# Optimization experiments

Measured on AMD Instinct MI355X. Metric: run time of the kernel, lower is better.

The kernel has to match this reference:

```python
import jax, jax.numpy as jnp
import numpy as np

N_NODES = 100000


def setup_inputs() -> dict:
    key = jax.random.key(0)
    ks = jax.random.split(key, 4)
    x = jax.random.normal(ks[0], (N_NODES, 128), dtype=jnp.float32)
    edge_index = jax.random.randint(ks[1], (2, 1600000), 0, N_NODES, dtype=jnp.int64)
    W1 = jax.random.normal(ks[2], (128, 64), dtype=jnp.float32) * (1.0 / np.sqrt(128))
    b1 = jnp.zeros((64,), dtype=jnp.float32)
    W2 = jax.random.normal(ks[3], (64, 64), dtype=jnp.float32) * (1.0 / np.sqrt(64))
    b2 = jnp.zeros((64,), dtype=jnp.float32)
    return {"x": x, "edge_index": edge_index, "W1": W1, "b1": b1, "W2": W2, "b2": b2}


def reference(x, edge_index, W1, b1, W2, b2):
    N = x.shape[0]
    loop = jnp.arange(N, dtype=edge_index.dtype)
    src = jnp.concatenate([edge_index[0], loop])  # [E+N] sources (incl. self-loops)
    dst = jnp.concatenate([edge_index[1], loop])  # [E+N] targets
    # symmetric GCN normalization: deg counts edge weights (all 1) at target nodes
    deg = jax.ops.segment_sum(jnp.ones_like(src, dtype=x.dtype), dst, num_segments=N)
    dinv = jnp.where(deg > 0, jax.lax.rsqrt(deg), 0.0)
    norm = (dinv[src] * dinv[dst])[:, None]  # [E+N, 1]

    def gcn_conv(h, W, b):
        h = h @ W                                   # dense transform [N, out]
        msg = h[src] * norm                         # gather + normalize [E+N, out]
        agg = jax.ops.segment_sum(msg, dst, num_segments=N)  # scatter-add
        return agg + b

    h = jax.nn.gelu(gcn_conv(x, W1, b1), approximate=False)  # torch nn.GELU = exact erf
    return gcn_conv(h, W2, b2)
```

## Files before the change

kernel.cpp:

```cpp
#include <hip/hip_runtime.h>
#include <math.h>

#define N_NODES 100000
#define N_EDGES 1600000
#define NROWS 100032
#define NBUK 782
#define BCAP 2600
#define BINCHUNK 4096

typedef unsigned short u16;
typedef u16 u16x4 __attribute__((ext_vector_type(4)));
typedef u16 u16x8 __attribute__((ext_vector_type(8)));
typedef short s16x8 __attribute__((ext_vector_type(8)));
typedef float f32x4 __attribute__((ext_vector_type(4)));

__device__ __forceinline__ float bf2f(u16 u) {
    union { unsigned i; float f; } v; v.i = ((unsigned)u) << 16; return v.f;
}
__device__ __forceinline__ u16 f2bf(float f) {
    union { float f; unsigned i; } v; v.f = f;
    return (u16)((v.i + 0x7FFFu + ((v.i >> 16) & 1u)) >> 16);
}

__global__ __launch_bounds__(256) void k_bin(const int* __restrict__ src,
                                             const int* __restrict__ dst,
                                             int* bucketCursor,
                                             unsigned int* __restrict__ bins) {
    __shared__ int lcnt[NBUK];
    __shared__ int lbase[NBUK];
    const int t = threadIdx.x;
    for (int i = t; i < NBUK; i += 256) lcnt[i] = 0;
    __syncthreads();

    const int e0 = blockIdx.x * BINCHUNK + t * 16;
    int4 s4[4], d4[4];
    int bkt[16], rnk[16];
    const bool valid = e0 < N_EDGES;
    if (valid) {
        #pragma unroll
        for (int k = 0; k < 4; ++k) {
            s4[k] = *(const int4*)(src + e0 + 4 * k);
            d4[k] = *(const int4*)(dst + e0 + 4 * k);
        }
        #pragma unroll
        for (int k = 0; k < 4; ++k) {
            int dd[4] = { d4[k].x, d4[k].y, d4[k].z, d4[k].w };
            #pragma unroll
            for (int j = 0; j < 4; ++j) {
                int b = dd[j] >> 7;
                bkt[4 * k + j] = b;
                rnk[4 * k + j] = atomicAdd(&lcnt[b], 1);
            }
        }
    }
    __syncthreads();
    for (int i = t; i < NBUK; i += 256)
        if (lcnt[i] > 0) lbase[i] = atomicAdd(&bucketCursor[i], lcnt[i]);
    __syncthreads();
    if (valid) {
        #pragma unroll
        for (int k = 0; k < 4; ++k) {
            int ss[4] = { s4[k].x, s4[k].y, s4[k].z, s4[k].w };
            int dd[4] = { d4[k].x, d4[k].y, d4[k].z, d4[k].w };
            #pragma unroll
            for (int j = 0; j < 4; ++j) {
                int i = 4 * k + j;
                unsigned w = ((unsigned)(dd[j] & 127) << 17) | (unsigned)ss[j];
                bins[(size_t)bkt[i] * BCAP + lbase[bkt[i]] + rnk[i]] = w;
            }
        }
    }
}

__global__ __launch_bounds__(256) void k_bscan(const int* __restrict__ bucketCursor,
                                               int* __restrict__ gBase,
                                               int* __restrict__ row_start) {
    __shared__ int sd[256];
    const int t = threadIdx.x;
    const int idx0 = t * 4;
    int v0 = (idx0 + 0 < NBUK) ? bucketCursor[idx0 + 0] : 0;
    int v1 = (idx0 + 1 < NBUK) ? bucketCursor[idx0 + 1] : 0;
    int v2 = (idx0 + 2 < NBUK) ? bucketCursor[idx0 + 2] : 0;
    int v3 = (idx0 + 3 < NBUK) ? bucketCursor[idx0 + 3] : 0;
    int s0 = v0, s1 = s0 + v1, s2 = s1 + v2, s3 = s2 + v3;
    sd[t] = s3;
    __syncthreads();
    #pragma unroll
    for (int off = 1; off < 256; off <<= 1) {
        int x = (t >= off) ? sd[t - off] : 0;
        __syncthreads();
        sd[t] += x;
        __syncthreads();
    }
    int excl = (t > 0) ? sd[t - 1] : 0;
    if (idx0 + 0 < NBUK) gBase[idx0 + 0] = excl;
    if (idx0 + 1 < NBUK) gBase[idx0 + 1] = excl + s0;
    if (idx0 + 2 < NBUK) gBase[idx0 + 2] = excl + s1;
    if (idx0 + 3 < NBUK) gBase[idx0 + 3] = excl + s2;
    if (t == 0) row_start[N_NODES] = N_EDGES;
}

__global__ __launch_bounds__(256) void k_build(const unsigned int* __restrict__ bins,
                                               const int* __restrict__ bucketCursor,
                                               const int* __restrict__ gBase,
                                               int* __restrict__ row_start,
                                               float* __restrict__ dinv,
                                               int* __restrict__ csr_src) {
    __shared__ int cnt[128];
    __shared__ int ps[128];
    __shared__ int cur[128];
    const int b = blockIdx.x;
    const int t = threadIdx.x;
    const int bcnt = bucketCursor[b];
    const int gb = gBase[b];
    const unsigned int* mybins = bins + (size_t)b * BCAP;

    if (t < 128) cnt[t] = 0;
    __syncthreads();
    for (int i = t; i < bcnt; i += 256)
        atomicAdd(&cnt[mybins[i] >> 17], 1);
    __syncthreads();
    if (t < 128) ps[t] = cnt[t];
    __syncthreads();
    #pragma unroll
    for (int off = 1; off < 128; off <<= 1) {
        int x = (t >= off && t < 128) ? ps[t - off] : 0;
        __syncthreads();
        if (t < 128) ps[t] += x;
        __syncthreads();
    }
    if (t < 128) {
        int excl = (t > 0) ? ps[t - 1] : 0;
        cur[t] = excl;
        int node = (b << 7) + t;
        if (node < N_NODES) {
            row_start[node] = gb + excl;
            dinv[node] = rsqrtf((float)(cnt[t] + 1));
        }
    }
    __syncthreads();
    for (int i = t; i < bcnt; i += 256) {
        unsigned w = mybins[i];
        int dl = w >> 17;
        int s = (int)(w & 0x1FFFFu);
        int p = atomicAdd(&cur[dl], 1);
        csr_src[gb + p] = s;
    }
}

__global__ __launch_bounds__(256) void k_wsplit(const float* __restrict__ W1,
                                                const float* __restrict__ W2,
                                                u16* __restrict__ w1pre,
                                                u16* __restrict__ w2pre) {
    const int t = threadIdx.x;
    const int b = blockIdx.x;
    if (b < 16) {
        #pragma unroll
        for (int half = 0; half < 2; ++half) {
            int e = b * 512 + half * 256 + t;
            int k = e >> 6, c = e & 63;
            float f = W1[e];
            u16 h = f2bf(f);
            u16 l = f2bf(f - bf2f(h));
            int byte = (c * 256 + k * 2) ^ ((c & 7) << 4);
            *(u16*)((char*)w1pre + byte) = h;
            *(u16*)((char*)w1pre + 16384 + byte) = l;
        }
    } else {
        int e = (b - 16) * 256 + t;
        int k = e >> 6, c = e & 63;
        float f = W2[e];
        u16 h = f2bf(f);
        u16 l = f2bf(f - bf2f(h));
        int byte = (c * 128 + k * 2) ^ ((c & 7) << 4);
        *(u16*)((char*)w2pre + byte) = h;
        *(u16*)((char*)w2pre + 8192 + byte) = l;
    }
}

__device__ __forceinline__ void quant_store_row(float v0, float v1, float v2, float v3,
                                                int row, int l16,
                                                signed char* __restrict__ H8,
                                                float* __restrict__ scale) {
    float m = fmaxf(fmaxf(fabsf(v0), fabsf(v1)), fmaxf(fabsf(v2), fabsf(v3)));
    m = fmaxf(m, __shfl_xor(m, 1));
    m = fmaxf(m, __shfl_xor(m, 2));
    m = fmaxf(m, __shfl_xor(m, 4));
    m = fmaxf(m, __shfl_xor(m, 8));
    float inv = (m > 0.f) ? 127.f / m : 0.f;
    if (l16 == 0) scale[row] = m * (1.f / 127.f);
    size_t base = (size_t)row * 64 + l16;
    H8[base +  0] = (signed char)__float2int_rn(v0 * inv);
    H8[base + 16] = (signed char)__float2int_rn(v1 * inv);
    H8[base + 32] = (signed char)__float2int_rn(v2 * inv);
    H8[base + 48] = (signed char)__float2int_rn(v3 * inv);
}

__global__ __launch_bounds__(256) void k_gemm1(const float* __restrict__ X,
                                               const u16* __restrict__ w1pre,
                                               const float* __restrict__ dinv,
                                               signed char* __restrict__ H8,
                                               float* __restrict__ scale) {
    __shared__ u16 sxh[64 * 128];
    __shared__ u16 sxl[64 * 128];
    __shared__ u16 wth[64 * 128];
    __shared__ u16 wtl[64 * 128];
    const int t = threadIdx.x;
    const int blk = blockIdx.x;

    {
        const float4* Xv = (const float4*)X;
        #pragma unroll
        for (int i = 0; i < 8; ++i) {
            int idx = i * 256 + t;
            int row = idx >> 5;
            int k4  = (idx & 31) << 2;
            int grow = blk * 64 + row;
            float4 v = make_float4(0.f, 0.f, 0.f, 0.f);
            if (grow < N_NODES) v = Xv[(size_t)grow * 32 + (idx & 31)];
            float f[4] = { v.x, v.y, v.z, v.w };
            u16x4 hv, lv;
            #pragma unroll
            for (int j = 0; j < 4; ++j) {
                u16 h = f2bf(f[j]);
                hv[j] = h;
                lv[j] = f2bf(f[j] - bf2f(h));
            }
            int byte = (row * 256 + k4 * 2) ^ ((row & 7) << 4);
            *(u16x4*)((char*)sxh + byte) = hv;
            *(u16x4*)((char*)sxl + byte) = lv;
        }
    }
    {
        const u16x8* G = (const u16x8*)w1pre;
        u16x8* Lh = (u16x8*)wth;
        u16x8* Ll = (u16x8*)wtl;
        #pragma unroll
        for (int i = 0; i < 4; ++i) Lh[i * 256 + t] = G[i * 256 + t];
        #pragma unroll
        for (int i = 0; i < 4; ++i) Ll[i * 256 + t] = G[1024 + i * 256 + t];
    }
    __syncthreads();

    const int lane = t & 63;
    const int w    = t >> 6;
    const int l16  = lane & 15;
    const int kg   = lane >> 4;
    f32x4 acc[4];
    #pragma unroll
    for (int nt = 0; nt < 4; ++nt)
        #pragma unroll
        for (int j = 0; j < 4; ++j) acc[nt][j] = 0.f;

    const int arow = w * 16 + l16;
    const int aswz = (arow & 7) << 4;
    #pragma unroll
    for (int kt = 0; kt < 4; ++kt) {
        const int koff = kt * 64 + kg * 16;
        s16x8 ah = *(const s16x8*)((const char*)sxh + ((arow * 256 + koff) ^ aswz));
        s16x8 al = *(const s16x8*)((const char*)sxl + ((arow * 256 + koff) ^ aswz));
        #pragma unroll
        for (int nt = 0; nt < 4; ++nt) {
            const int c = nt * 16 + l16;
            const int wb = (c * 256 + koff) ^ ((c & 7) << 4);
            s16x8 bh = *(const s16x8*)((const char*)wth + wb);
            s16x8 bl = *(const s16x8*)((const char*)wtl + wb);
            acc[nt] = __builtin_amdgcn_mfma_f32_16x16x32_bf16(ah, bh, acc[nt], 0, 0, 0);
            acc[nt] = __builtin_amdgcn_mfma_f32_16x16x32_bf16(ah, bl, acc[nt], 0, 0, 0);
            acc[nt] = __builtin_amdgcn_mfma_f32_16x16x32_bf16(al, bh, acc[nt], 0, 0, 0);
        }
    }
    const int rbase = blk * 64 + w * 16 + kg * 4;
    #pragma unroll
    for (int reg = 0; reg < 4; ++reg) {
        int row = rbase + reg;
        float di = (row < N_NODES) ? dinv[row] : 0.f;
        quant_store_row(acc[0][reg] * di, acc[1][reg] * di,
                        acc[2][reg] * di, acc[3][reg] * di,
                        row, l16, H8, scale);
    }
}

__global__ __launch_bounds__(256) void k_gemm2(const u16* __restrict__ Xb,
                                               const u16* __restrict__ w2pre,
                                               const float* __restrict__ dinv,
                                               signed char* __restrict__ H8,
                                               float* __restrict__ scale) {
    __shared__ u16 sxb[64 * 64];
    __shared__ u16 wth[64 * 64];
    __shared__ u16 wtl[64 * 64];
    const int t = threadIdx.x;
    const int blk = blockIdx.x;

    {
        const u16x8* Xv = (const u16x8*)Xb;
        #pragma unroll
        for (int i = 0; i < 2; ++i) {
            int idx = i * 256 + t;
            int row = idx >> 3;
            int k0  = (idx & 7) << 3;
            int grow = blk * 64 + row;
            u16x8 v;
            #pragma unroll
            for (int j = 0; j < 8; ++j) v[j] = 0;
            if (grow < N_NODES) v = Xv[(size_t)grow * 8 + (idx & 7)];
            int byte = (row * 128 + k0 * 2) ^ ((row & 7) << 4);
            *(u16x8*)((char*)sxb + byte) = v;
        }
    }
    {
        const u16x8* G = (const u16x8*)w2pre;
        u16x8* Lh = (u16x8*)wth;
        u16x8* Ll = (u16x8*)wtl;
        #pragma unroll
        for (int i = 0; i < 2; ++i) Lh[i * 256 + t] = G[i * 256 + t];
        #pragma unroll
        for (int i = 0; i < 2; ++i) Ll[i * 256 + t] = G[512 + i * 256 + t];
    }
    __syncthreads();

    const int lane = t & 63;
    const int w    = t >> 6;
    const int l16  = lane & 15;
    const int kg   = lane >> 4;
    f32x4 acc[4];
    #pragma unroll
    for (int nt = 0; nt < 4; ++nt)
        #pragma unroll
        for (int j = 0; j < 4; ++j) acc[nt][j] = 0.f;

    const int arow = w * 16 + l16;
    const int aswz = (arow & 7) << 4;
    #pragma unroll
    for (int kt = 0; kt < 2; ++kt) {
        const int koff = kt * 64 + kg * 16;
        s16x8 a = *(const s16x8*)((const char*)sxb + ((arow * 128 + koff) ^ aswz));
        #pragma unroll
        for (int nt = 0; nt < 4; ++nt) {
            const int c = nt * 16 + l16;
            const int wb = (c * 128 + koff) ^ ((c & 7) << 4);
            s16x8 bh = *(const s16x8*)((const char*)wth + wb);
            s16x8 bl = *(const s16x8*)((const char*)wtl + wb);
            acc[nt] = __builtin_amdgcn_mfma_f32_16x16x32_bf16(a, bh, acc[nt], 0, 0, 0);
            acc[nt] = __builtin_amdgcn_mfma_f32_16x16x32_bf16(a, bl, acc[nt], 0, 0, 0);
        }
    }
    const int rbase = blk * 64 + w * 16 + kg * 4;
    #pragma unroll
    for (int reg = 0; reg < 4; ++reg) {
        int row = rbase + reg;
        float di = (row < N_NODES) ? dinv[row] : 0.f;
        quant_store_row(acc[0][reg] * di, acc[1][reg] * di,
                        acc[2][reg] * di, acc[3][reg] * di,
                        row, l16, H8, scale);
    }
}

template <bool GELU>
__global__ __launch_bounds__(256) void k_aggregate(const signed char* __restrict__ hs8,
                                                   const float* __restrict__ scale,
                                                   const int* __restrict__ csr_src,
                                                   const int* __restrict__ row_start,
                                                   const float* __restrict__ dinv,
                                                   const float* __restrict__ b,
                                                   void* __restrict__ outraw) {
    const int t = threadIdx.x;
    const int lane = t & 63;
    const int node = __builtin_amdgcn_readfirstlane(blockIdx.x * 4 + (t >> 6));
    const int jS = __builtin_amdgcn_readfirstlane(row_start[node]);
    const int jE = __builtin_amdgcn_readfirstlane(row_start[node + 1]);
    const int deg = jE - jS;
    const signed char* __restrict__ colp = hs8 + lane;

    const int l32 = lane & 31;
    int rr = csr_src[jS + l32];
    int myIdx = (l32 < deg) ? rr : N_NODES;
    float myScale = scale[myIdx];

    float acc = (float)colp[(size_t)node << 6] * scale[node];

    signed char v[32];
    #pragma unroll
    for (int i = 0; i < 32; ++i) {
        int r = __builtin_amdgcn_readlane(myIdx, i);
        v[i] = colp[(size_t)(unsigned)r << 6];
    }
    #pragma unroll
    for (int i = 0; i < 32; ++i) {
        float s = __uint_as_float(__builtin_amdgcn_readlane(__float_as_uint(myScale), i));
        acc += (float)v[i] * s;
    }

    if (deg > 32) {
        for (int j = jS + 32; j < jE; ++j) {
            int r = __builtin_amdgcn_readfirstlane(csr_src[j]);
            float s = __uint_as_float(__builtin_amdgcn_readfirstlane(
                          __float_as_uint(scale[r])));
            acc += (float)colp[(size_t)(unsigned)r << 6] * s;
        }
    }

    float r = dinv[node] * acc + b[lane];
    if (GELU) {
        r = 0.5f * r * (1.0f + erff(r * 0.70710678118654752f));
        ((u16*)outraw)[((size_t)node << 6) + lane] = f2bf(r);
    } else {
        ((float*)outraw)[((size_t)node << 6) + lane] = r;
    }
}

extern "C" void kernel_launch(void* const* d_in, const int* in_sizes, int n_in,
                              void* d_out, int out_size, void* d_ws, size_t ws_size,
                              hipStream_t stream) {
    const float* x  = (const float*)d_in[0];
    const int* edge = (const int*)d_in[1];
    const float* W1 = (const float*)d_in[2];
    const float* b1 = (const float*)d_in[3];
    const float* W2 = (const float*)d_in[4];
    const float* b2 = (const float*)d_in[5];
    float* out = (float*)d_out;

    const int* src = edge;
    const int* dst = edge + N_EDGES;

    char* ws = (char*)d_ws;
    int*   bucketCursor = (int*)(ws);
    int*   gBase        = (int*)(ws + 4096);
    int*   row_start    = (int*)(ws + 8192);
    float* dinv         = (float*)(ws + 408576);
    int*   csr_src      = (int*)(ws + 808960);
    float* scale1       = (float*)(ws + 7209216);
    float* scale2       = (float*)(ws + 7609344);
    signed char* hs8a   = (signed char*)(ws + 8009472);
    signed char* hs8b   = (signed char*)(ws + 14411520);
    u16*   out1b        = (u16*)(ws + 20813568);
    unsigned int* bins  = (unsigned int*)out1b;
    u16*   w1pre        = (u16*)(ws + 33617664);
    u16*   w2pre        = (u16*)(ws + 33650432);

    const int nBlkBin  = (N_EDGES + BINCHUNK - 1) / BINCHUNK;
    const int nBlkGemm = NROWS / 64;
    const int nBlkAgg  = N_NODES / 4;

    hipMemsetAsync(bucketCursor, 0, NBUK * sizeof(int), stream);
    k_wsplit<<<32, 256, 0, stream>>>(W1, W2, w1pre, w2pre);
    k_bin<<<nBlkBin, 256, 0, stream>>>(src, dst, bucketCursor, bins);
    k_bscan<<<1, 256, 0, stream>>>(bucketCursor, gBase, row_start);
    k_build<<<NBUK, 256, 0, stream>>>(bins, bucketCursor, gBase, row_start, dinv, csr_src);

    k_gemm1<<<nBlkGemm, 256, 0, stream>>>(x, w1pre, dinv, hs8a, scale1);
    k_aggregate<true><<<nBlkAgg, 256, 0, stream>>>(hs8a, scale1, csr_src, row_start, dinv, b1, out1b);

    k_gemm2<<<nBlkGemm, 256, 0, stream>>>(out1b, w2pre, dinv, hs8b, scale2);
    k_aggregate<false><<<nBlkAgg, 256, 0, stream>>>(hs8b, scale2, csr_src, row_start, dinv, b2, out);
}
```

Before: 160.8 us.

## Fuse edge binning with GEMM1 and drop bucket scan via atomic CSR offsets

Edge binning and the first GEMM now run in a single launch, with separate block ranges, so the two independent stages overlap. The bucket prefix scan and the memset are removed: each build block claims its CSR segment from a global atomic cursor, and zeroing of the cursors moves into the weight-split kernel. Because the GEMMs no longer need dinv, the source-side dinv scaling moves into the aggregation gather, which lets GEMM1 start before the CSR build. Row start and degree are packed into one word, which caps degree at 255 and adds a dinv gather per neighbor.

Measured after the change: 157.5 us. 2.1% less time.

```diff
diff --git a/kernel.cpp b/kernel.cpp
--- a/kernel.cpp
+++ b/kernel.cpp
@@ -7,6 +7,8 @@
 #define NBUK 782
 #define BCAP 2600
 #define BINCHUNK 4096
+#define NBINBLK 391
+#define NGEMMBLK 1563
 
 typedef unsigned short u16;
 typedef u16 u16x4 __attribute__((ext_vector_type(4)));
@@ -22,136 +24,13 @@
     return (u16)((v.i + 0x7FFFu + ((v.i >> 16) & 1u)) >> 16);
 }
 
-__global__ __launch_bounds__(256) void k_bin(const int* __restrict__ src,
-                                             const int* __restrict__ dst,
-                                             int* bucketCursor,
-                                             unsigned int* __restrict__ bins) {
-    __shared__ int lcnt[NBUK];
-    __shared__ int lbase[NBUK];
-    const int t = threadIdx.x;
-    for (int i = t; i < NBUK; i += 256) lcnt[i] = 0;
-    __syncthreads();
-
-    const int e0 = blockIdx.x * BINCHUNK + t * 16;
-    int4 s4[4], d4[4];
-    int bkt[16], rnk[16];
-    const bool valid = e0 < N_EDGES;
-    if (valid) {
-        #pragma unroll
-        for (int k = 0; k < 4; ++k) {
-            s4[k] = *(const int4*)(src + e0 + 4 * k);
-            d4[k] = *(const int4*)(dst + e0 + 4 * k);
-        }
-        #pragma unroll
-        for (int k = 0; k < 4; ++k) {
-            int dd[4] = { d4[k].x, d4[k].y, d4[k].z, d4[k].w };
-            #pragma unroll
-            for (int j = 0; j < 4; ++j) {
-                int b = dd[j] >> 7;
-                bkt[4 * k + j] = b;
-                rnk[4 * k + j] = atomicAdd(&lcnt[b], 1);
-            }
-        }
-    }
-    __syncthreads();
-    for (int i = t; i < NBUK; i += 256)
-        if (lcnt[i] > 0) lbase[i] = atomicAdd(&bucketCursor[i], lcnt[i]);
-    __syncthreads();
-    if (valid) {
-        #pragma unroll
-        for (int k = 0; k < 4; ++k) {
-            int ss[4] = { s4[k].x, s4[k].y, s4[k].z, s4[k].w };
-            int dd[4] = { d4[k].x, d4[k].y, d4[k].z, d4[k].w };
-            #pragma unroll
-            for (int j = 0; j < 4; ++j) {
-                int i = 4 * k + j;
-                unsigned w = ((unsigned)(dd[j] & 127) << 17) | (unsigned)ss[j];
-                bins[(size_t)bkt[i] * BCAP + lbase[bkt[i]] + rnk[i]] = w;
-            }
-        }
-    }
-}
-
-__global__ __launch_bounds__(256) void k_bscan(const int* __restrict__ bucketCursor,
-                                               int* __restrict__ gBase,
-                                               int* __restrict__ row_start) {
-    __shared__ int sd[256];
-    const int t = threadIdx.x;
-    const int idx0 = t * 4;
-    int v0 = (idx0 + 0 < NBUK) ? bucketCursor[idx0 + 0] : 0;
-    int v1 = (idx0 + 1 < NBUK) ? bucketCursor[idx0 + 1] : 0;
-    int v2 = (idx0 + 2 < NBUK) ? bucketCursor[idx0 + 2] : 0;
-    int v3 = (idx0 + 3 < NBUK) ? bucketCursor[idx0 + 3] : 0;
-    int s0 = v0, s1 = s0 + v1, s2 = s1 + v2, s3 = s2 + v3;
-    sd[t] = s3;
-    __syncthreads();
-    #pragma unroll
-    for (int off = 1; off < 256; off <<= 1) {
-        int x = (t >= off) ? sd[t - off] : 0;
-        __syncthreads();
-        sd[t] += x;
-        __syncthreads();
-    }
-    int excl = (t > 0) ? sd[t - 1] : 0;
-    if (idx0 + 0 < NBUK) gBase[idx0 + 0] = excl;
-    if (idx0 + 1 < NBUK) gBase[idx0 + 1] = excl + s0;
-    if (idx0 + 2 < NBUK) gBase[idx0 + 2] = excl + s1;
-    if (idx0 + 3 < NBUK) gBase[idx0 + 3] = excl + s2;
-    if (t == 0) row_start[N_NODES] = N_EDGES;
-}
-
-__global__ __launch_bounds__(256) void k_build(const unsigned int* __restrict__ bins,
-                                               const int* __restrict__ bucketCursor,
-                                               const int* __restrict__ gBase,
-                                               int* __restrict__ row_start,
-                                               float* __restrict__ dinv,
-                                               int* __restrict__ csr_src) {
-    __shared__ int cnt[128];
-    __shared__ int ps[128];
-    __shared__ int cur[128];
-    const int b = blockIdx.x;
-    const int t = threadIdx.x;
-    const int bcnt = bucketCursor[b];
-    const int gb = gBase[b];
-    const unsigned int* mybins = bins + (size_t)b * BCAP;
-
-    if (t < 128) cnt[t] = 0;
-    __syncthreads();
-    for (int i = t; i < bcnt; i += 256)
-        atomicAdd(&cnt[mybins[i] >> 17], 1);
-    __syncthreads();
-    if (t < 128) ps[t] = cnt[t];
-    __syncthreads();
-    #pragma unroll
-    for (int off = 1; off < 128; off <<= 1) {
-        int x = (t >= off && t < 128) ? ps[t - off] : 0;
-        __syncthreads();
-        if (t < 128) ps[t] += x;
-        __syncthreads();
-    }
-    if (t < 128) {
-        int excl = (t > 0) ? ps[t - 1] : 0;
-        cur[t] = excl;
-        int node = (b << 7) + t;
-        if (node < N_NODES) {
-            row_start[node] = gb + excl;
-            dinv[node] = rsqrtf((float)(cnt[t] + 1));
-        }
-    }
-    __syncthreads();
-    for (int i = t; i < bcnt; i += 256) {
-        unsigned w = mybins[i];
-        int dl = w >> 17;
-        int s = (int)(w & 0x1FFFFu);
-        int p = atomicAdd(&cur[dl], 1);
-        csr_src[gb + p] = s;
-    }
-}
-
-__global__ __launch_bounds__(256) void k_wsplit(const float* __restrict__ W1,
-                                                const float* __restrict__ W2,
-                                                u16* __restrict__ w1pre,
-                                                u16* __restrict__ w2pre) {
+__global__ __launch_bounds__(256) void k_pre(const float* __restrict__ W1,
+                                             const float* __restrict__ W2,
+                                             u16* __restrict__ w1pre,
+                                             u16* __restrict__ w2pre,
+                                             int* __restrict__ bucketCursor,
+                                             int* __restrict__ totalCursor,
+                                             float* __restrict__ dinv) {
     const int t = threadIdx.x;
     const int b = blockIdx.x;
     if (b < 16) {
@@ -175,6 +54,10 @@
         int byte = (c * 128 + k * 2) ^ ((c & 7) << 4);
         *(u16*)((char*)w2pre + byte) = h;
         *(u16*)((char*)w2pre + 8192 + byte) = l;
+    }
+    if (b == 0) {
+        for (int i = t; i < NBUK; i += 256) bucketCursor[i] = 0;
+        if (t == 0) { totalCursor[0] = 0; dinv[N_NODES] = 0.f; }
     }
 }
 
@@ -196,17 +79,69 @@
     H8[base + 48] = (signed char)__float2int_rn(v3 * inv);
 }
 
-__global__ __launch_bounds__(256) void k_gemm1(const float* __restrict__ X,
-                                               const u16* __restrict__ w1pre,
-                                               const float* __restrict__ dinv,
-                                               signed char* __restrict__ H8,
-                                               float* __restrict__ scale) {
-    __shared__ u16 sxh[64 * 128];
-    __shared__ u16 sxl[64 * 128];
-    __shared__ u16 wth[64 * 128];
-    __shared__ u16 wtl[64 * 128];
+__global__ __launch_bounds__(256) void k_bin_gemm1(const int* __restrict__ src,
+                                                   const int* __restrict__ dst,
+                                                   int* bucketCursor,
+                                                   unsigned int* __restrict__ bins,
+                                                   const float* __restrict__ X,
+                                                   const u16* __restrict__ w1pre,
+                                                   signed char* __restrict__ H8,
+                                                   float* __restrict__ scale) {
+    __shared__ __align__(16) char smem[65536];
     const int t = threadIdx.x;
-    const int blk = blockIdx.x;
+
+    if (blockIdx.x < NBINBLK) {
+        int* lcnt  = (int*)smem;
+        int* lbase = (int*)(smem + 4096);
+        for (int i = t; i < NBUK; i += 256) lcnt[i] = 0;
+        __syncthreads();
+
+        const int e0 = blockIdx.x * BINCHUNK + t * 16;
+        int4 s4[4], d4[4];
+        int bkt[16], rnk[16];
+        const bool valid = e0 < N_EDGES;
+        if (valid) {
+            #pragma unroll
+            for (int k = 0; k < 4; ++k) {
+                s4[k] = *(const int4*)(src + e0 + 4 * k);
+                d4[k] = *(const int4*)(dst + e0 + 4 * k);
+            }
+            #pragma unroll
+            for (int k = 0; k < 4; ++k) {
+                int dd[4] = { d4[k].x, d4[k].y, d4[k].z, d4[k].w };
+                #pragma unroll
+                for (int j = 0; j < 4; ++j) {
+                    int b = dd[j] >> 7;
+                    bkt[4 * k + j] = b;
+                    rnk[4 * k + j] = atomicAdd(&lcnt[b], 1);
+                }
+            }
+        }
+        __syncthreads();
+        for (int i = t; i < NBUK; i += 256)
+            if (lcnt[i] > 0) lbase[i] = atomicAdd(&bucketCursor[i], lcnt[i]);
+        __syncthreads();
+        if (valid) {
+            #pragma unroll
+            for (int k = 0; k < 4; ++k) {
+                int ss[4] = { s4[k].x, s4[k].y, s4[k].z, s4[k].w };
+                int dd[4] = { d4[k].x, d4[k].y, d4[k].z, d4[k].w };
+                #pragma unroll
+                for (int j = 0; j < 4; ++j) {
+                    int i = 4 * k + j;
+                    unsigned w = ((unsigned)(dd[j] & 127) << 17) | (unsigned)ss[j];
+                    bins[(size_t)bkt[i] * BCAP + lbase[bkt[i]] + rnk[i]] = w;
+                }
+            }
+        }
+        return;
+    }
+
+    u16* sxh = (u16*)smem;
+    u16* sxl = (u16*)(smem + 16384);
+    u16* wth = (u16*)(smem + 32768);
+    u16* wtl = (u16*)(smem + 49152);
+    const int blk = blockIdx.x - NBINBLK;
 
     {
         const float4* Xv = (const float4*)X;
@@ -274,16 +209,63 @@
     #pragma unroll
     for (int reg = 0; reg < 4; ++reg) {
         int row = rbase + reg;
-        float di = (row < N_NODES) ? dinv[row] : 0.f;
-        quant_store_row(acc[0][reg] * di, acc[1][reg] * di,
-                        acc[2][reg] * di, acc[3][reg] * di,
+        quant_store_row(acc[0][reg], acc[1][reg], acc[2][reg], acc[3][reg],
                         row, l16, H8, scale);
+    }
+}
+
+__global__ __launch_bounds__(256) void k_build(const unsigned int* __restrict__ bins,
+                                               const int* __restrict__ bucketCursor,
+                                               int* totalCursor,
+                                               unsigned int* __restrict__ rowPack,
+                                               float* __restrict__ dinv,
+                                               int* __restrict__ csr_src) {
+    __shared__ int cnt[128];
+    __shared__ int ps[128];
+    __shared__ int cur[128];
+    __shared__ int gbS;
+    const int b = blockIdx.x;
+    const int t = threadIdx.x;
+    const int bcnt = bucketCursor[b];
+    const unsigned int* mybins = bins + (size_t)b * BCAP;
+
+    if (t == 0) gbS = atomicAdd(totalCursor, bcnt);
+    if (t < 128) cnt[t] = 0;
+    __syncthreads();
+    for (int i = t; i < bcnt; i += 256)
+        atomicAdd(&cnt[mybins[i] >> 17], 1);
+    __syncthreads();
+    if (t < 128) ps[t] = cnt[t];
+    __syncthreads();
+    #pragma unroll
+    for (int off = 1; off < 128; off <<= 1) {
+        int x = (t >= off && t < 128) ? ps[t - off] : 0;
+        __syncthreads();
+        if (t < 128) ps[t] += x;
+        __syncthreads();
+    }
+    const int gb = gbS;
+    if (t < 128) {
+        int excl = (t > 0) ? ps[t - 1] : 0;
+        cur[t] = excl;
+        int node = (b << 7) + t;
+        if (node < N_NODES) {
+            rowPack[node] = ((unsigned)(gb + excl) << 8) | (unsigned)cnt[t];
+            dinv[node] = rsqrtf((float)(cnt[t] + 1));
+        }
+    }
+    __syncthreads();
+    for (int i = t; i < bcnt; i += 256) {
+        unsigned w = mybins[i];
+        int dl = w >> 17;
+        int s = (int)(w & 0x1FFFFu);
+        int p = atomicAdd(&cur[dl], 1);
+        csr_src[gb + p] = s;
     }
 }
 
 __global__ __launch_bounds__(256) void k_gemm2(const u16* __restrict__ Xb,
                                                const u16* __restrict__ w2pre,
-                                               const float* __restrict__ dinv,
                                                signed char* __restrict__ H8,
                                                float* __restrict__ scale) {
     __shared__ u16 sxb[64 * 64];
@@ -349,9 +331,7 @@
     #pragma unroll
     for (int reg = 0; reg < 4; ++reg) {
         int row = rbase + reg;
-        float di = (row < N_NODES) ? dinv[row] : 0.f;
-        quant_store_row(acc[0][reg] * di, acc[1][reg] * di,
-                        acc[2][reg] * di, acc[3][reg] * di,
+        quant_store_row(acc[0][reg], acc[1][reg], acc[2][reg], acc[3][reg],
                         row, l16, H8, scale);
     }
 }
@@ -359,25 +339,26 @@
 template <bool GELU>
 __global__ __launch_bounds__(256) void k_aggregate(const signed char* __restrict__ hs8,
                                                    const float* __restrict__ scale,
+                                                   const float* __restrict__ dinv,
                                                    const int* __restrict__ csr_src,
-                                                   const int* __restrict__ row_start,
-                                                   const float* __restrict__ dinv,
+                                                   const unsigned int* __restrict__ rowPack,
                                                    const float* __restrict__ b,
                                                    void* __restrict__ outraw) {
     const int t = threadIdx.x;
     const int lane = t & 63;
     const int node = __builtin_amdgcn_readfirstlane(blockIdx.x * 4 + (t >> 6));
-    const int jS = __builtin_amdgcn_readfirstlane(row_start[node]);
-    const int jE = __builtin_amdgcn_readfirstlane(row_start[node + 1]);
-    const int deg = jE - jS;
+    const unsigned u = __builtin_amdgcn_readfirstlane(rowPack[node]);
+    const int jS  = (int)(u >> 8);
+    const int deg = (int)(u & 255u);
     const signed char* __restrict__ colp = hs8 + lane;
 
     const int l32 = lane & 31;
     int rr = csr_src[jS + l32];
     int myIdx = (l32 < deg) ? rr : N_NODES;
-    float myScale = scale[myIdx];
-
-    float acc = (float)colp[(size_t)node << 6] * scale[node];
+    float myS = scale[myIdx] * dinv[myIdx];
+
+    const float dn = dinv[node];
+    float acc = (float)colp[(size_t)node << 6] * (scale[node] * dn);
 
     signed char v[32];
     #pragma unroll
@@ -387,20 +368,20 @@
     }
     #pragma unroll
     for (int i = 0; i < 32; ++i) {
-        float s = __uint_as_float(__builtin_amdgcn_readlane(__float_as_uint(myScale), i));
+        float s = __uint_as_float(__builtin_amdgcn_readlane(__float_as_uint(myS), i));
         acc += (float)v[i] * s;
     }
 
     if (deg > 32) {
-        for (int j = jS + 32; j < jE; ++j) {
+        for (int j = jS + 32; j < jS + deg; ++j) {
             int r = __builtin_amdgcn_readfirstlane(csr_src[j]);
             float s = __uint_as_float(__builtin_amdgcn_readfirstlane(
-                          __float_as_uint(scale[r])));
+                          __float_as_uint(scale[r] * dinv[r])));
             acc += (float)colp[(size_t)(unsigned)r << 6] * s;
         }
     }
 
-    float r = dinv[node] * acc + b[lane];
+    float r = dn * acc + b[lane];
     if (GELU) {
         r = 0.5f * r * (1.0f + erff(r * 0.70710678118654752f));
         ((u16*)outraw)[((size_t)node << 6) + lane] = f2bf(r);
@@ -424,33 +405,27 @@
     const int* dst = edge + N_EDGES;
 
     char* ws = (char*)d_ws;
-    int*   bucketCursor = (int*)(ws);
-    int*   gBase        = (int*)(ws + 4096);
-    int*   row_start    = (int*)(ws + 8192);
-    float* dinv         = (float*)(ws + 408576);
-    int*   csr_src      = (int*)(ws + 808960);
-    float* scale1       = (float*)(ws + 7209216);
-    float* scale2       = (float*)(ws + 7609344);
-    signed char* hs8a   = (signed char*)(ws + 8009472);
-    signed char* hs8b   = (signed char*)(ws + 14411520);
-    u16*   out1b        = (u16*)(ws + 20813568);
-    unsigned int* bins  = (unsigned int*)out1b;
-    u16*   w1pre        = (u16*)(ws + 33617664);
-    u16*   w2pre        = (u16*)(ws + 33650432);
-
-    const int nBlkBin  = (N_EDGES + BINCHUNK - 1) / BINCHUNK;
-    const int nBlkGemm = NROWS / 64;
-    const int nBlkAgg  = N_NODES / 4;
-
-    hipMemsetAsync(bucketCursor, 0, NBUK * sizeof(int), stream);
-    k_wsplit<<<32, 256, 0, stream>>>(W1, W2, w1pre, w2pre);
-    k_bin<<<nBlkBin, 256, 0, stream>>>(src, dst, bucketCursor, bins);
-    k_bscan<<<1, 256, 0, stream>>>(bucketCursor, gBase, row_start);
-    k_build<<<NBUK, 256, 0, stream>>>(bins, bucketCursor, gBase, row_start, dinv, csr_src);
-
-    k_gemm1<<<nBlkGemm, 256, 0, stream>>>(x, w1pre, dinv, hs8a, scale1);
-    k_aggregate<true><<<nBlkAgg, 256, 0, stream>>>(hs8a, scale1, csr_src, row_start, dinv, b1, out1b);
-
-    k_gemm2<<<nBlkGemm, 256, 0, stream>>>(out1b, w2pre, dinv, hs8b, scale2);
-    k_aggregate<false><<<nBlkAgg, 256, 0, stream>>>(hs8b, scale2, csr_src, row_start, dinv, b2, out);
-}
+    int*      bucketCursor = (int*)(ws);
+    int*      totalCursor  = (int*)(ws + 4096);
+    unsigned* rowPack      = (unsigned*)(ws + 8192);
+    float*    dinv         = (float*)(ws + 408576);
+    int*      csr_src      = (int*)(ws + 808960);
+    float*    scale1       = (float*)(ws + 7209216);
+    float*    scale2       = (float*)(ws + 7609344);
+    signed char* hs8a      = (signed char*)(ws + 8009472);
+    signed char* hs8b      = (signed char*)(ws + 14411520);
+    u16*      out1b        = (u16*)(ws + 20813568);
+    unsigned* bins         = (unsigned*)out1b;
+    u16*      w1pre        = (u16*)(ws + 33617664);
+    u16*      w2pre        = (u16*)(ws + 33650432);
+
+    const int nBlkAgg = N_NODES / 4;
+
+    k_pre<<<32, 256, 0, stream>>>(W1, W2, w1pre, w2pre, bucketCursor, totalCursor, dinv);
+    k_bin_gemm1<<<NBINBLK + NGEMMBLK, 256, 0, stream>>>(src, dst, bucketCursor, bins,
+                                                        x, w1pre, hs8a, scale1);
+    k_build<<<NBUK, 256, 0, stream>>>(bins, bucketCursor, totalCursor, rowPack, dinv, csr_src);
+    k_aggregate<true><<<nBlkAgg, 256, 0, stream>>>(hs8a, scale1, dinv, csr_src, rowPack, b1, out1b);
+    k_gemm2<<<NGEMMBLK, 256, 0, stream>>>(out1b, w2pre, hs8b, scale2);
+    k_aggregate<false><<<nBlkAgg, 256, 0, stream>>>(hs8b, scale2, dinv, csr_src, rowPack, b2, out);
+}
```
